# Kernel tuning notes

Measured on AMD Instinct MI355X. Metric: run time of the kernel, lower is better.

The kernel has to match this reference:

```python
import jax, jax.numpy as jnp
import numpy as np

B, T, C, U = 256, 512, 512, 512  # batch, timesteps, n_in, units


def setup_inputs() -> dict:
    key = jax.random.key(0)
    k1, k2, k3, k4 = jax.random.split(key, 4)
    x = jax.random.normal(k1, (B, T, C), dtype=jnp.float32)
    dones = (jax.random.uniform(k2, (B, T, 1)) < 0.05).astype(jnp.float32)
    # keras 'uniform' initializer default range is [-0.05, 0.05]
    wx = jax.random.uniform(k3, (C, 4 * U), jnp.float32, -0.05, 0.05)
    wh = jax.random.uniform(k4, (U, 4 * U), jnp.float32, -0.05, 0.05)
    b = jnp.zeros((4 * U,), jnp.float32)
    return {"x": x, "dones": dones, "wx": wx, "wh": wh, "b": b}


def reference(x, dones, wx, wh, b):
    # x: [B,T,C], dones: [B,T,1], wx: [C,4U], wh: [U,4U], b: [4U]
    Bn, Tn, Cn = x.shape
    Un = wh.shape[0]

    def step(carry, xt):
        c, h = carry                     # [B,U] each
        xi, dt = xt                      # xi: [B,C], dt: [B,1]
        keep = 1.0 - dt
        c = c * keep
        h = h * keep
        z = xi @ wx + h @ wh + b         # [B,4U]
        i, f, o, u = jnp.split(z, 4, axis=-1)
        i = jax.nn.sigmoid(i)
        f = jax.nn.sigmoid(f)
        o = jax.nn.sigmoid(o)
        u = jnp.tanh(u)
        c = f * c + i * u
        h = o * jnp.tanh(c)
        return (c, h), h

    c0 = jnp.zeros((Bn, Un), x.dtype)   # self.states starts at zeros
    h0 = jnp.zeros((Bn, Un), x.dtype)
    (c, h), hs = jax.lax.scan(step, (c0, h0), (x.transpose(1, 0, 2), dones.transpose(1, 0, 2)))
    xs = hs.transpose(1, 0, 2)          # [B,T,U] (return_sequence=True)
    s = jnp.concatenate([c, h], axis=-1)  # [B,2U] (squeezed final state)
    return xs, s
```

## Files before the change

kernel.cpp:

```cpp
#include <hip/hip_runtime.h>

#define BATCH 256
#define TT 512
#define CIN 512
#define UU 512
#define ZN 2048
#define BT (BATCH*TT)
#define NWGPB 16

typedef __attribute__((ext_vector_type(8))) short short8;
typedef __attribute__((ext_vector_type(4))) float f32x4;

__device__ __forceinline__ short f2bf(float f){
  unsigned u = __float_as_uint(f);
  u += 0x7fffu + ((u >> 16) & 1u);
  return (short)(u >> 16);
}
__device__ __forceinline__ float bf2f(unsigned short s){
  unsigned u = ((unsigned)s) << 16;
  return __uint_as_float(u);
}

#define GLD16(g, l) __builtin_amdgcn_global_load_lds( \
    (const __attribute__((address_space(1))) void*)(g), \
    (__attribute__((address_space(3))) void*)(l), 16, 0, 0)

#define CLOAD(dst, p, OFFSTR) asm volatile( \
    "global_load_dwordx4 %0, %1, off offset:" OFFSTR " sc0 sc1" \
    : "=v"(dst) : "v"(p) : "memory")
#define CLOADW(dst, p) asm volatile( \
    "global_load_dword %0, %1, off sc0 sc1" \
    : "=v"(dst) : "v"(p) : "memory")

__device__ __forceinline__ void st_coh_u16(void* p, unsigned v){
  asm volatile("global_store_short %0, %1, off sc0 sc1" :: "v"(p), "v"(v) : "memory");
}
__device__ __forceinline__ void st_coh_u32(void* p, unsigned v){
  asm volatile("global_store_dword %0, %1, off sc0 sc1" :: "v"(p), "v"(v) : "memory");
}

__device__ __forceinline__ float sigm(float x){ return 1.0f/(1.0f + __expf(-x)); }
__device__ __forceinline__ float tanh_fast(float x){ return 1.0f - 2.0f/(1.0f + __expf(2.0f*x)); }

__global__ __launch_bounds__(256) void convert_x_kernel(const float* __restrict__ x,
                                                        short* __restrict__ xb){
  const long total = (long)TT*BATCH*64;
  const long stride = (long)gridDim.x * blockDim.x;
  for (long i = (long)blockIdx.x * blockDim.x + threadIdx.x; i < total; i += stride){
    const int c8 = (int)(i & 63);
    const long tb = i >> 6;
    const int b = (int)(tb & (BATCH-1));
    const int t = (int)(tb >> 8);
    const float* src = x + ((long)b*TT + t)*CIN + c8*8;
    const float4 v0 = *(const float4*)(src);
    const float4 v1 = *(const float4*)(src + 4);
    short8 o;
    o[0]=f2bf(v0.x); o[1]=f2bf(v0.y); o[2]=f2bf(v0.z); o[3]=f2bf(v0.w);
    o[4]=f2bf(v1.x); o[5]=f2bf(v1.y); o[6]=f2bf(v1.z); o[7]=f2bf(v1.w);
    *(short8*)(xb + i*8) = o;
  }
}

__global__ __launch_bounds__(256) void transpose_w_kernel(
    const float* __restrict__ wx, const float* __restrict__ wh,
    short* __restrict__ wxt, short* __restrict__ wht){
  const float* src = blockIdx.z ? wh : wx;
  short* dst = blockIdx.z ? wht : wxt;
  __shared__ float tile[32][33];
  const int nt = blockIdx.x << 5;
  const int kt = blockIdx.y << 5;
  const int tx = threadIdx.x & 31, ty = threadIdx.x >> 5;
  #pragma unroll
  for (int i = 0; i < 32; i += 8)
    tile[ty+i][tx] = src[(long)(kt+ty+i)*ZN + nt+tx];
  __syncthreads();
  #pragma unroll
  for (int i = 0; i < 32; i += 8)
    dst[(long)(nt+ty+i)*512 + kt+tx] = f2bf(tile[tx][ty+i]);
}

__global__ __launch_bounds__(256) void gemm_xpart_kernel(
    const short* __restrict__ A, const short* __restrict__ Bt,
    const float* __restrict__ bias, short* __restrict__ Co){
  __shared__ short As[128*32];
  __shared__ short Bs[128*32];
  const int wg = blockIdx.x;
  const int xcd = wg & 7;
  const int ii = wg >> 3;
  const long m0 = (long)(xcd*128 + (ii >> 4)) << 7;
  const long n0 = (long)(ii & 15) << 7;
  const int tid = threadIdx.x;
  const int lane = tid & 63;
  const int wave = tid >> 6;
  const int wm = wave & 1, wn = wave >> 1;
  f32x4 acc[4][4] = {};
  const int srow = tid >> 2;
  const int sseg = tid & 3;
  const long aoff = (m0 + srow) * 512 + sseg * 8;
  const long boff = (n0 + srow) * 512 + sseg * 8;
  short* ldsa = &As[tid * 8];
  short* ldsb = &Bs[tid * 8];
  for (int k0 = 0; k0 < 512; k0 += 32){
    __syncthreads();
    GLD16(A + aoff + k0, ldsa);
    GLD16(A + aoff + 64*512 + k0, ldsa + 2048);
    GLD16(Bt + boff + k0, ldsb);
    GLD16(Bt + boff + 64*512 + k0, ldsb + 2048);
    __syncthreads();
    const int kb = (lane >> 4) * 8;
    short8 af[4], bf[4];
    #pragma unroll
    for (int mi = 0; mi < 4; mi++) af[mi] = *(const short8*)&As[(wm*64 + mi*16 + (lane&15))*32 + kb];
    #pragma unroll
    for (int ni = 0; ni < 4; ni++) bf[ni] = *(const short8*)&Bs[(wn*64 + ni*16 + (lane&15))*32 + kb];
    #pragma unroll
    for (int mi = 0; mi < 4; mi++)
      #pragma unroll
      for (int ni = 0; ni < 4; ni++)
        acc[mi][ni] = __builtin_amdgcn_mfma_f32_16x16x32_bf16(af[mi], bf[ni], acc[mi][ni], 0, 0, 0);
  }
  #pragma unroll
  for (int ni = 0; ni < 4; ni++){
    const long col = n0 + wn*64 + ni*16 + (lane & 15);
    const float bv = bias[col];
    #pragma unroll
    for (int mi = 0; mi < 4; mi++){
      const long row = m0 + wm*64 + mi*16 + ((lane >> 4) << 2);
      #pragma unroll
      for (int r = 0; r < 4; r++)
        Co[(row + r)*ZN + col] = f2bf(acc[mi][ni][r] + bv);
    }
  }
}

__global__ __launch_bounds__(512, 2) void lstm_persist_kernel(
    const short* __restrict__ xpart, const float* __restrict__ dones,
    const short* __restrict__ wht, short* __restrict__ hb0,
    short* __restrict__ hb1, unsigned* __restrict__ flags,
    float* __restrict__ out){
  __shared__ short h_lds[8192];
  __shared__ float zpart[128*19 + 16];
  const int tid = threadIdx.x;
  const int lane = tid & 63;
  const int wv = tid >> 6;
  const int bg = blockIdx.x & 15;
  const int cg = blockIdx.x >> 4;
  const int rb = bg << 4;
  const int uc = cg << 5;
  const int j = lane & 15;
  const int hq = lane >> 4;
  const int g_w = wv >> 1;
  const int ucl = ((wv & 1) << 4) + j;
  const int zl = g_w*32 + ucl;

  short8 bfr[16];
  {
    const short* wsrc = wht + ((long)(g_w*512 + uc + ucl))*512 + hq*8;
    #pragma unroll
    for (int m = 0; m < 16; m++)
      bfr[m] = *(const short8*)(wsrc + m*32);
  }

  const int srow = tid >> 5;
  const int scol = (tid & 31) << 4;
  const int swb = (srow << 10) + (scol << 1);
  const int sxor = (srow & 7) << 4;
  const int arb = (j << 10) + (hq << 4);
  const int axor = (j & 7) << 4;

  const int erow = tid >> 5;
  const int euj  = tid & 31;
  const int eucol = uc + euj;
  const int row  = rb + erow;

  unsigned* fl = flags + bg*16;
  const unsigned short* xp16 = (const unsigned short*)xpart;

  float c = 0.0f;
  float dn;
  unsigned short xp[4];
  dn = dones[(long)row*TT + 0];
  #pragma unroll
  for (int g = 0; g < 4; g++)
    xp[g] = xp16[((long)0*BATCH + row)*ZN + (g<<9) + eucol];

  for (int t = 0; t < TT; t++){
    {
      const short* hsrc = ((t & 1) ? hb1 : hb0) + (long)(rb + srow)*UU + scol;
      short8 hv0, hv1;
      CLOAD(hv0, hsrc, "0");
      CLOAD(hv1, hsrc, "16");
      asm volatile("s_waitcnt vmcnt(0)" ::: "memory");
      *(short8*)((char*)h_lds + ( swb       ^ sxor)) = hv0;
      *(short8*)((char*)h_lds + ((swb + 16) ^ sxor)) = hv1;
    }
    __syncthreads();
    short8 a[16];
    #pragma unroll
    for (int m = 0; m < 16; m++)
      a[m] = *(const short8*)((const char*)h_lds + ((arb + (m << 6)) ^ axor));
    f32x4 acc0 = {}, acc1 = {};
    #pragma unroll
    for (int m = 0; m < 16; m += 2){
      acc0 = __builtin_amdgcn_mfma_f32_16x16x32_bf16(a[m],   bfr[m],   acc0, 0, 0, 0);
      acc1 = __builtin_amdgcn_mfma_f32_16x16x32_bf16(a[m+1], bfr[m+1], acc1, 0, 0, 0);
    }
    const f32x4 acc = acc0 + acc1;
    #pragma unroll
    for (int r = 0; r < 4; r++)
      zpart[zl*19 + hq*4 + r] = acc[r];
    __syncthreads();
    const float keep = 1.0f - dn;
    const float cold = c * keep;
    const float z0 = bf2f(xp[0]) + keep*zpart[(0*32 + euj)*19 + erow];
    const float z1 = bf2f(xp[1]) + keep*zpart[(1*32 + euj)*19 + erow];
    const float z2 = bf2f(xp[2]) + keep*zpart[(2*32 + euj)*19 + erow];
    const float z3 = bf2f(xp[3]) + keep*zpart[(3*32 + euj)*19 + erow];
    const float gi = sigm(z0);
    const float gf = sigm(z1);
    const float go = sigm(z2);
    const float gu = tanh_fast(z3);
    const float cn = gf*cold + gi*gu;
    const float hn = go * tanh_fast(cn);
    c = cn;
    if (t == TT-1){
      out[(long)row*TT*UU + (long)t*UU + eucol] = hn;
      float* s = out + (long)BATCH*TT*UU;
      s[(long)row*2*UU + eucol] = cn;
      s[(long)row*2*UU + UU + eucol] = hn;
    } else {
      short* hdst = (t & 1) ? hb0 : hb1;
      st_coh_u16(hdst + (long)row*UU + eucol, (unsigned)(unsigned short)f2bf(hn));
      asm volatile("s_waitcnt vmcnt(0)" ::: "memory");
      __syncthreads();
      if (tid == 0) st_coh_u32(fl + cg, (unsigned)(t+1));
      out[(long)row*TT*UU + (long)t*UU + eucol] = hn;
      dn = dones[(long)row*TT + (t+1)];
      #pragma unroll
      for (int g = 0; g < 4; g++)
        xp[g] = xp16[((long)(t+1)*BATCH + row)*ZN + (g<<9) + eucol];
      if (wv == 0){
        const unsigned tgt = (unsigned)(t+1);
        unsigned v;
        for (;;){
          CLOADW(v, fl + (lane & 15));
          asm volatile("s_waitcnt vmcnt(0)" ::: "memory");
          if (__all((int)(v >= tgt))) break;
          __builtin_amdgcn_s_sleep(1);
        }
      }
      __syncthreads();
    }
  }
}

extern "C" void kernel_launch(void* const* d_in, const int* in_sizes, int n_in,
                              void* d_out, int out_size, void* d_ws, size_t ws_size,
                              hipStream_t stream){
  const float* x     = (const float*)d_in[0];
  const float* dones = (const float*)d_in[1];
  const float* wx    = (const float*)d_in[2];
  const float* wh    = (const float*)d_in[3];
  const float* b     = (const float*)d_in[4];
  float* out = (float*)d_out;
  char* ws = (char*)d_ws;
  short* x_tb  = (short*)(ws);
  short* wx_t  = (short*)(ws + 134217728L);
  short* wh_t  = (short*)(ws + 136314880L);
  short* xpart = (short*)(ws + 138412032L);
  short* hb0   = (short*)(ws + 675282944L);
  short* hb1   = (short*)(ws + 675545088L);
  unsigned* flags = (unsigned*)(ws + 675807232L);

  hipMemsetAsync(hb0, 0, 262144, stream);
  hipMemsetAsync(flags, 0, 1024, stream);
  convert_x_kernel<<<2048, 256, 0, stream>>>(x, x_tb);
  transpose_w_kernel<<<dim3(64,16,2), 256, 0, stream>>>(wx, wh, wx_t, wh_t);
  gemm_xpart_kernel<<<16384, 256, 0, stream>>>(x_tb, wx_t, b, xpart);
  lstm_persist_kernel<<<256, 512, 0, stream>>>(xpart, dones, wh_t, hb0, hb1, flags, out);
}
```

Baseline: 1.856 ms.

## Replace flag barrier with timestep-tagged hidden state words for per-element sync

Each hidden value is now stored as a 32-bit word holding the bf16 value and the timestep tag, and consumers spin on the tagged data itself. This removes the separate flag store, the store-drain wait, an extra block barrier and the flag polling loop. The LDS layout for h is also changed so the MFMA A operands are read with simple linear addressing instead of XOR-swizzled loads. In exchange, h traffic doubles in bytes, every thread now polls global memory, and launch bounds drop to 1 block per CU.

```diff
diff --git a/kernel.cpp b/kernel.cpp
--- a/kernel.cpp
+++ b/kernel.cpp
@@ -6,10 +6,10 @@
 #define UU 512
 #define ZN 2048
 #define BT (BATCH*TT)
-#define NWGPB 16
 
 typedef __attribute__((ext_vector_type(8))) short short8;
 typedef __attribute__((ext_vector_type(4))) float f32x4;
+typedef __attribute__((ext_vector_type(4))) unsigned u32x4;
 
 __device__ __forceinline__ short f2bf(float f){
   unsigned u = __float_as_uint(f);
@@ -28,13 +28,7 @@
 #define CLOAD(dst, p, OFFSTR) asm volatile( \
     "global_load_dwordx4 %0, %1, off offset:" OFFSTR " sc0 sc1" \
     : "=v"(dst) : "v"(p) : "memory")
-#define CLOADW(dst, p) asm volatile( \
-    "global_load_dword %0, %1, off sc0 sc1" \
-    : "=v"(dst) : "v"(p) : "memory")
-
-__device__ __forceinline__ void st_coh_u16(void* p, unsigned v){
-  asm volatile("global_store_short %0, %1, off sc0 sc1" :: "v"(p), "v"(v) : "memory");
-}
+
 __device__ __forceinline__ void st_coh_u32(void* p, unsigned v){
   asm volatile("global_store_dword %0, %1, off sc0 sc1" :: "v"(p), "v"(v) : "memory");
 }
@@ -133,11 +127,10 @@
   }
 }
 
-__global__ __launch_bounds__(512, 2) void lstm_persist_kernel(
+__global__ __launch_bounds__(512, 1) void lstm_persist_kernel(
     const short* __restrict__ xpart, const float* __restrict__ dones,
-    const short* __restrict__ wht, short* __restrict__ hb0,
-    short* __restrict__ hb1, unsigned* __restrict__ flags,
-    float* __restrict__ out){
+    const short* __restrict__ wht, unsigned* __restrict__ ht0,
+    unsigned* __restrict__ ht1, float* __restrict__ out){
   __shared__ short h_lds[8192];
   __shared__ float zpart[128*19 + 16];
   const int tid = threadIdx.x;
@@ -161,49 +154,63 @@
       bfr[m] = *(const short8*)(wsrc + m*32);
   }
 
-  const int srow = tid >> 5;
-  const int scol = (tid & 31) << 4;
-  const int swb = (srow << 10) + (scol << 1);
-  const int sxor = (srow & 7) << 4;
-  const int arb = (j << 10) + (hq << 4);
-  const int axor = (j & 7) << 4;
+  const int srow = tid & 15;
+  const int skg  = tid >> 4;
+  const long hoff = (long)(rb + srow)*UU + skg*16;
+  short* sdst = h_lds + skg*256 + srow*8;
 
   const int erow = tid >> 5;
   const int euj  = tid & 31;
   const int eucol = uc + euj;
   const int row  = rb + erow;
 
-  unsigned* fl = flags + bg*16;
   const unsigned short* xp16 = (const unsigned short*)xpart;
 
   float c = 0.0f;
   float dn;
   unsigned short xp[4];
-  dn = dones[(long)row*TT + 0];
+  dn = dones[(long)row*TT];
   #pragma unroll
   for (int g = 0; g < 4; g++)
-    xp[g] = xp16[((long)0*BATCH + row)*ZN + (g<<9) + eucol];
+    xp[g] = xp16[(long)row*ZN + (g<<9) + eucol];
 
   for (int t = 0; t < TT; t++){
     {
-      const short* hsrc = ((t & 1) ? hb1 : hb0) + (long)(rb + srow)*UU + scol;
-      short8 hv0, hv1;
-      CLOAD(hv0, hsrc, "0");
-      CLOAD(hv1, hsrc, "16");
-      asm volatile("s_waitcnt vmcnt(0)" ::: "memory");
-      *(short8*)((char*)h_lds + ( swb       ^ sxor)) = hv0;
-      *(short8*)((char*)h_lds + ((swb + 16) ^ sxor)) = hv1;
-    }
-    __syncthreads();
-    short8 a[16];
-    #pragma unroll
-    for (int m = 0; m < 16; m++)
-      a[m] = *(const short8*)((const char*)h_lds + ((arb + (m << 6)) ^ axor));
+      const unsigned* hs = ((t & 1) ? ht1 : ht0) + hoff;
+      const unsigned tg = (unsigned)t;
+      u32x4 w0, w1, w2, w3;
+      for (;;){
+        CLOAD(w0, hs, "0"); CLOAD(w1, hs, "16");
+        CLOAD(w2, hs, "32"); CLOAD(w3, hs, "48");
+        asm volatile("s_waitcnt vmcnt(0)" ::: "memory");
+        const unsigned d = (w0[0]^tg)|(w0[1]^tg)|(w0[2]^tg)|(w0[3]^tg)
+                         | (w1[0]^tg)|(w1[1]^tg)|(w1[2]^tg)|(w1[3]^tg)
+                         | (w2[0]^tg)|(w2[1]^tg)|(w2[2]^tg)|(w2[3]^tg)
+                         | (w3[0]^tg)|(w3[1]^tg)|(w3[2]^tg)|(w3[3]^tg);
+        if (__all((int)((d & 0xffffu) == 0u))) break;
+        __builtin_amdgcn_s_sleep(1);
+      }
+      u32x4 pa, pb;
+      pa[0] = (w0[0]>>16) | (w0[1] & 0xffff0000u);
+      pa[1] = (w0[2]>>16) | (w0[3] & 0xffff0000u);
+      pa[2] = (w1[0]>>16) | (w1[1] & 0xffff0000u);
+      pa[3] = (w1[2]>>16) | (w1[3] & 0xffff0000u);
+      pb[0] = (w2[0]>>16) | (w2[1] & 0xffff0000u);
+      pb[1] = (w2[2]>>16) | (w2[3] & 0xffff0000u);
+      pb[2] = (w3[0]>>16) | (w3[1] & 0xffff0000u);
+      pb[3] = (w3[2]>>16) | (w3[3] & 0xffff0000u);
+      *(u32x4*)(sdst)       = pa;
+      *(u32x4*)(sdst + 128) = pb;
+    }
+    __syncthreads();
+    const short* abase = h_lds + lane*8;
     f32x4 acc0 = {}, acc1 = {};
     #pragma unroll
     for (int m = 0; m < 16; m += 2){
-      acc0 = __builtin_amdgcn_mfma_f32_16x16x32_bf16(a[m],   bfr[m],   acc0, 0, 0, 0);
-      acc1 = __builtin_amdgcn_mfma_f32_16x16x32_bf16(a[m+1], bfr[m+1], acc1, 0, 0, 0);
+      const short8 a0 = *(const short8*)(abase + m*512);
+      const short8 a1 = *(const short8*)(abase + m*512 + 512);
+      acc0 = __builtin_amdgcn_mfma_f32_16x16x32_bf16(a0, bfr[m],   acc0, 0, 0, 0);
+      acc1 = __builtin_amdgcn_mfma_f32_16x16x32_bf16(a1, bfr[m+1], acc1, 0, 0, 0);
     }
     const f32x4 acc = acc0 + acc1;
     #pragma unroll
@@ -229,27 +236,15 @@
       s[(long)row*2*UU + eucol] = cn;
       s[(long)row*2*UU + UU + eucol] = hn;
     } else {
-      short* hdst = (t & 1) ? hb0 : hb1;
-      st_coh_u16(hdst + (long)row*UU + eucol, (unsigned)(unsigned short)f2bf(hn));
-      asm volatile("s_waitcnt vmcnt(0)" ::: "memory");
-      __syncthreads();
-      if (tid == 0) st_coh_u32(fl + cg, (unsigned)(t+1));
+      unsigned* hd = (t & 1) ? ht0 : ht1;
+      const unsigned hv = ((unsigned)(unsigned short)f2bf(hn) << 16) | (unsigned)(t+1);
+      st_coh_u32(hd + (long)row*UU + eucol, hv);
       out[(long)row*TT*UU + (long)t*UU + eucol] = hn;
       dn = dones[(long)row*TT + (t+1)];
+      const long xb = ((long)(t+1)*BATCH + row)*ZN + eucol;
       #pragma unroll
       for (int g = 0; g < 4; g++)
-        xp[g] = xp16[((long)(t+1)*BATCH + row)*ZN + (g<<9) + eucol];
-      if (wv == 0){
-        const unsigned tgt = (unsigned)(t+1);
-        unsigned v;
-        for (;;){
-          CLOADW(v, fl + (lane & 15));
-          asm volatile("s_waitcnt vmcnt(0)" ::: "memory");
-          if (__all((int)(v >= tgt))) break;
-          __builtin_amdgcn_s_sleep(1);
-        }
-      }
-      __syncthreads();
+        xp[g] = xp16[xb + (g<<9)];
     }
   }
 }
@@ -268,14 +263,13 @@
   short* wx_t  = (short*)(ws + 134217728L);
   short* wh_t  = (short*)(ws + 136314880L);
   short* xpart = (short*)(ws + 138412032L);
-  short* hb0   = (short*)(ws + 675282944L);
-  short* hb1   = (short*)(ws + 675545088L);
-  unsigned* flags = (unsigned*)(ws + 675807232L);
-
-  hipMemsetAsync(hb0, 0, 262144, stream);
-  hipMemsetAsync(flags, 0, 1024, stream);
+  unsigned* ht0 = (unsigned*)(ws + 675282944L);
+  unsigned* ht1 = (unsigned*)(ws + 675807232L);
+
+  hipMemsetAsync(ht0, 0, 524288, stream);
+  hipMemsetAsync(ht1, 0, 524288, stream);
   convert_x_kernel<<<2048, 256, 0, stream>>>(x, x_tb);
   transpose_w_kernel<<<dim3(64,16,2), 256, 0, stream>>>(wx, wh, wx_t, wh_t);
   gemm_xpart_kernel<<<16384, 256, 0, stream>>>(x_tb, wx_t, b, xpart);
-  lstm_persist_kernel<<<256, 512, 0, stream>>>(xpart, dones, wh_t, hb0, hb1, flags, out);
-}
+  lstm_persist_kernel<<<256, 512, 0, stream>>>(xpart, dones, wh_t, ht0, ht1, out);
+}
```

Result: faster. 1.755 ms (-5.5%).
